# Kernel optimization log

Hardware: AMD Instinct MI355X
Metric: run time of the kernel (lower is better)

Reference implementation:

```python
import jax, jax.numpy as jnp
import numpy as np

B, T, N = 32, 64, 36
VD, H, S = 2048, 512, 300


def setup_inputs() -> dict:
    key = jax.random.key(0)
    ks = jax.random.split(key, 24)
    sc = 0.02
    d = {
        "visual": jax.random.normal(ks[0], (B, T, VD), jnp.float32),
        "objects": jax.random.normal(ks[1], (B, N, H), jnp.float32),
        # linear_layer
        "lin_W": jax.random.normal(ks[2], (H, VD), jnp.float32) * sc,
        "lin_b": jnp.zeros((H,), jnp.float32),
        # W, U projections
        "W_W": jax.random.normal(ks[3], (H, H), jnp.float32) * sc,
        "W_b": jnp.zeros((H,), jnp.float32),
        "U_W": jax.random.normal(ks[4], (H, H), jnp.float32) * sc,
        "U_b": jnp.zeros((H,), jnp.float32),
        # additive attention bias (torch.ones init)
        "b_attn": jnp.ones((H,), jnp.float32),
        # scoring vector w: Linear(H, 1)
        "w_W": jax.random.normal(ks[5], (1, H), jnp.float32) * sc,
        "w_b": jnp.zeros((1,), jnp.float32),
        # BiLSTM: input 2H, hidden H//2 per direction; gate order i,f,g,o
        "Wih_f": jax.random.normal(ks[6], (4 * (H // 2), 2 * H), jnp.float32) * sc,
        "Whh_f": jax.random.normal(ks[7], (4 * (H // 2), H // 2), jnp.float32) * sc,
        "bih_f": jnp.zeros((4 * (H // 2),), jnp.float32),
        "bhh_f": jnp.zeros((4 * (H // 2),), jnp.float32),
        "Wih_b": jax.random.normal(ks[8], (4 * (H // 2), 2 * H), jnp.float32) * sc,
        "Whh_b": jax.random.normal(ks[9], (4 * (H // 2), H // 2), jnp.float32) * sc,
        "bih_b": jnp.zeros((4 * (H // 2),), jnp.float32),
        "bhh_b": jnp.zeros((4 * (H // 2),), jnp.float32),
        # fc_layer
        "fc_W": jax.random.normal(ks[10], (S, H), jnp.float32) * sc,
        "fc_b": jnp.zeros((S,), jnp.float32),
    }
    return d


def _lstm(x, Wih, Whh, b):
    """Unidirectional LSTM over time. x: [B, T, D] -> [B, T, Hc]."""
    bsz = x.shape[0]
    Hc = Whh.shape[1]

    def step(carry, xt):
        h, c = carry
        g = xt @ Wih.T + h @ Whh.T + b          # [B, 4Hc]
        i, f, gg, o = jnp.split(g, 4, axis=-1)  # torch gate order i,f,g,o
        c = jax.nn.sigmoid(f) * c + jax.nn.sigmoid(i) * jnp.tanh(gg)
        h = jax.nn.sigmoid(o) * jnp.tanh(c)
        return (h, c), h

    h0 = jnp.zeros((bsz, Hc), x.dtype)
    _, hs = jax.lax.scan(step, (h0, h0), jnp.swapaxes(x, 0, 1))
    return jnp.swapaxes(hs, 0, 1)


def reference(visual, objects, lin_W, lin_b, W_W, W_b, U_W, U_b, b_attn,
              w_W, w_b, Wih_f, Whh_f, bih_f, bhh_f, Wih_b, Whh_b, bih_b,
              bhh_b, fc_W, fc_b):
    f3d = visual @ lin_W.T + lin_b                 # [B, T, H]
    Wf = f3d @ W_W.T + W_b                         # [B, T, H]
    Uo = objects @ U_W.T + U_b                     # [B, N, H]
    # broadcast additive attention: [B, T, N, H]
    attn_feat = Wf[:, :, None, :] + Uo[:, None, :, :] + b_attn
    scores = jnp.tanh(attn_feat) @ w_W.T + w_b     # [B, T, N, 1]
    attn_w = jax.nn.softmax(scores, axis=-2)       # softmax over objects N
    attn_obj = (attn_w * attn_feat).sum(axis=-2)   # [B, T, H]
    feats = jnp.concatenate([f3d, attn_obj], axis=-1)  # [B, T, 2H]
    out_f = _lstm(feats, Wih_f, Whh_f, bih_f + bhh_f)
    out_b = _lstm(feats[:, ::-1, :], Wih_b, Whh_b, bih_b + bhh_b)[:, ::-1, :]
    output = jnp.concatenate([out_f, out_b], axis=-1)  # [B, T, H]
    action = jnp.max(output, axis=1)                   # [B, H]
    action_semantics = action @ fc_W.T + fc_b          # [B, S]
    return output, action_semantics
```

## Files before the change

kernel.cpp:

```cpp
#include <hip/hip_runtime.h>
#include <hip/hip_bf16.h>
#include <type_traits>


typedef __hip_bfloat16 bf16;
typedef unsigned int uint32;
typedef __attribute__((ext_vector_type(8))) short s8v;
typedef __attribute__((ext_vector_type(4))) float f4v;
typedef __attribute__((ext_vector_type(4))) int   i32x4;

__device__ inline f4v mfma16(s8v a, s8v b, f4v c) {
    return __builtin_amdgcn_mfma_f32_16x16x32_bf16(a, b, c, 0, 0, 0);
}
__device__ inline float sigf(float x) {
    return __builtin_amdgcn_rcpf(1.f + __expf(-x));
}
__device__ inline float tanh_(float x) {
    return 1.f - 2.f * __builtin_amdgcn_rcpf(1.f + __expf(2.f * x));
}
__device__ inline void gload_lds16(const bf16* g, bf16* l) {
    __builtin_amdgcn_global_load_lds(
        (const __attribute__((address_space(1))) void*)g,
        (__attribute__((address_space(3))) void*)l, 16, 0, 0);
}

struct CvtJobs {
    const float* src[9];
    bf16*        dst[9];
    int          start[10];
};

__global__ __launch_bounds__(256) void cvt_kernel(CvtJobs jobs) {
    int blk = blockIdx.x;
    int j = 0;
#pragma unroll
    for (int i = 1; i < 9; ++i) if (blk >= jobs.start[i]) j = i;
    int off = (blk - jobs.start[j]) * 1024 + threadIdx.x * 4;
    float4 v = *(const float4*)(jobs.src[j] + off);
    union { bf16 h[4]; uint2 u; } p;
    p.h[0] = __float2bfloat16(v.x);
    p.h[1] = __float2bfloat16(v.y);
    p.h[2] = __float2bfloat16(v.z);
    p.h[3] = __float2bfloat16(v.w);
    *(uint2*)(jobs.dst[j] + off) = p.u;
}

template <typename CT>
__global__ __launch_bounds__(256) void gemm_tile(
    const bf16* __restrict__ A, int lda,
    const bf16* __restrict__ W,
    const float* __restrict__ b1, const float* __restrict__ b2,
    CT* __restrict__ C, int ldc,
    int K, int tiles_n, int permuteTB)
{
    __shared__ bf16 As[128 * 64];
    __shared__ bf16 Bs[128 * 64];

    int tid = threadIdx.x;
    int w = tid >> 6, lane = tid & 63;
    int lo = lane & 15, hi = lane >> 4;
    int mt = blockIdx.x / tiles_n, nt = blockIdx.x % tiles_n;
    int wm = w >> 1, wn = w & 1;

    const bf16* Ab = A + (size_t)(mt * 128) * lda;
    const bf16* Wb = W + (size_t)(nt * 128) * K;

    f4v acc[4][4];
#pragma unroll
    for (int m = 0; m < 4; ++m)
#pragma unroll
        for (int n = 0; n < 4; ++n) acc[m][n] = (f4v){0.f, 0.f, 0.f, 0.f};

    int wbase = tid & 192;

    for (int k0 = 0; k0 < K; k0 += 64) {
#pragma unroll
        for (int i = 0; i < 4; ++i) {
            int ci = i * 256 + tid;
            int row = ci >> 3, c = ci & 7;
            int gc = c ^ (row & 7);
            gload_lds16(Ab + (size_t)row * lda + k0 + gc * 8,
                        As + (i * 256 + wbase) * 8);
            gload_lds16(Wb + (size_t)row * K + k0 + gc * 8,
                        Bs + (i * 256 + wbase) * 8);
        }
        __syncthreads();

#pragma unroll
        for (int kt = 0; kt < 2; ++kt) {
            s8v a[4], b[4];
            int sw = ((kt * 4 + hi) ^ (lo & 7)) * 8;
#pragma unroll
            for (int m = 0; m < 4; ++m)
                a[m] = *(const s8v*)(As + (wm * 64 + m * 16 + lo) * 64 + sw);
#pragma unroll
            for (int n = 0; n < 4; ++n)
                b[n] = *(const s8v*)(Bs + (wn * 64 + n * 16 + lo) * 64 + sw);
#pragma unroll
            for (int m = 0; m < 4; ++m)
#pragma unroll
                for (int n = 0; n < 4; ++n)
                    acc[m][n] = mfma16(a[m], b[n], acc[m][n]);
        }
        __syncthreads();
    }

#pragma unroll
    for (int n = 0; n < 4; ++n) {
        int cc = nt * 128 + wn * 64 + n * 16 + lo;
        float bv = (b1 ? b1[cc] : 0.f) + (b2 ? b2[cc] : 0.f);
#pragma unroll
        for (int m = 0; m < 4; ++m) {
            int rbase = mt * 128 + wm * 64 + m * 16 + hi * 4;
#pragma unroll
            for (int i = 0; i < 4; ++i) {
                int r = rbase + i;
                int rr = permuteTB ? ((r & 63) * 32 + (r >> 6)) : r;
                float v = acc[m][n][i] + bv;
                if constexpr (std::is_same<CT, float>::value)
                    C[(size_t)rr * ldc + cc] = v;
                else
                    C[(size_t)rr * ldc + cc] = __float2bfloat16(v);
            }
        }
    }
}

__global__ __launch_bounds__(256) void attn_kernel(
    const float* __restrict__ Wf,
    const float* __restrict__ Uo,
    const float* __restrict__ wW,
    const float* __restrict__ wB,
    bf16* __restrict__ feats)
{
    int bt = blockIdx.x, b = bt >> 6;
    int wv = threadIdx.x >> 6, lane = threadIdx.x & 63;
    __shared__ float s_aw[36];

    float wfr[8], wr[8];
    const float* wfrow = Wf + (size_t)bt * 512 + lane * 8;
#pragma unroll
    for (int i = 0; i < 8; ++i) {
        wfr[i] = wfrow[i];
        wr[i]  = wW[lane * 8 + i];
    }
    float wbv = wB[0];

    for (int n = wv; n < 36; n += 4) {
        const float* uo = Uo + ((size_t)b * 36 + n) * 512 + lane * 8;
        float s = 0.f;
#pragma unroll
        for (int i = 0; i < 8; ++i) s += wr[i] * tanh_(wfr[i] + uo[i]);
#pragma unroll
        for (int off = 32; off; off >>= 1) s += __shfl_xor(s, off);
        if (lane == 0) s_aw[n] = s + wbv;
    }
    __syncthreads();
    if (threadIdx.x == 0) {
        float mx = -1e30f;
#pragma unroll
        for (int n = 0; n < 36; ++n) mx = fmaxf(mx, s_aw[n]);
        float e[36], sum = 0.f;
#pragma unroll
        for (int n = 0; n < 36; ++n) { e[n] = __expf(s_aw[n] - mx); sum += e[n]; }
        float r = __builtin_amdgcn_rcpf(sum);
#pragma unroll
        for (int n = 0; n < 36; ++n) s_aw[n] = e[n] * r;
    }
    __syncthreads();

    int h0 = threadIdx.x * 2;
    const float* wf2 = Wf + (size_t)bt * 512 + h0;
    float a0 = wf2[0], a1 = wf2[1];
    for (int n = 0; n < 36; ++n) {
        float awn = s_aw[n];
        const float* uo = Uo + ((size_t)b * 36 + n) * 512 + h0;
        a0 += awn * uo[0];
        a1 += awn * uo[1];
    }
    feats[(size_t)bt * 1024 + 512 + h0]     = __float2bfloat16(a0);
    feats[(size_t)bt * 1024 + 512 + h0 + 1] = __float2bfloat16(a1);
}

__device__ inline void poll4(const int* p, int need) {
    for (;;) {
        i32x4 f;
        asm volatile("global_load_dwordx4 %0, %1, off sc1\n\t"
                     "s_waitcnt vmcnt(0)"
                     : "=v"(f) : "v"(p) : "memory");
        if (f[0] >= need && f[1] >= need && f[2] >= need && f[3] >= need)
            break;
    }
}

__device__ inline void load_h16(const uint32* pF, const uint32* pB, s8v* aF) {
    asm volatile(
        "global_load_dwordx4 %0, %16, off sc1\n\t"
        "global_load_dwordx4 %1, %16, off offset:64 sc1\n\t"
        "global_load_dwordx4 %2, %16, off offset:128 sc1\n\t"
        "global_load_dwordx4 %3, %16, off offset:192 sc1\n\t"
        "global_load_dwordx4 %4, %16, off offset:256 sc1\n\t"
        "global_load_dwordx4 %5, %16, off offset:320 sc1\n\t"
        "global_load_dwordx4 %6, %16, off offset:384 sc1\n\t"
        "global_load_dwordx4 %7, %16, off offset:448 sc1\n\t"
        "global_load_dwordx4 %8, %17, off sc1\n\t"
        "global_load_dwordx4 %9, %17, off offset:64 sc1\n\t"
        "global_load_dwordx4 %10, %17, off offset:128 sc1\n\t"
        "global_load_dwordx4 %11, %17, off offset:192 sc1\n\t"
        "global_load_dwordx4 %12, %17, off offset:256 sc1\n\t"
        "global_load_dwordx4 %13, %17, off offset:320 sc1\n\t"
        "global_load_dwordx4 %14, %17, off offset:384 sc1\n\t"
        "global_load_dwordx4 %15, %17, off offset:448 sc1\n\t"
        "s_waitcnt vmcnt(0)"
        : "=v"(aF[0]), "=v"(aF[1]), "=v"(aF[2]), "=v"(aF[3]),
          "=v"(aF[4]), "=v"(aF[5]), "=v"(aF[6]), "=v"(aF[7]),
          "=v"(aF[8]), "=v"(aF[9]), "=v"(aF[10]), "=v"(aF[11]),
          "=v"(aF[12]), "=v"(aF[13]), "=v"(aF[14]), "=v"(aF[15])
        : "v"(pF), "v"(pB)
        : "memory");
}

__global__ __launch_bounds__(256, 1) void lstm_kernel(
    const bf16* __restrict__ WhhF, const bf16* __restrict__ WhhB,
    const float* __restrict__ gatesF, const float* __restrict__ gatesB,
    uint32* __restrict__ hx,
    float* __restrict__ out,
    int* __restrict__ bar)
{
    int bi  = blockIdx.x;
    int g   = bi >> 2;
    int pid = bi & 3;
    int jb  = pid * 64;
    int wv = threadIdx.x >> 6, lane = threadIdx.x & 63;
    int lo = lane & 15, hi = lane >> 4;
    int j0 = jb + wv * 16;

    uint32* hxg  = hx + (size_t)g * 8192;
    int*    flags = bar + g * 16;

    s8v whh[2][4][8];
#pragma unroll
    for (int q = 0; q < 4; ++q)
#pragma unroll
        for (int kt = 0; kt < 8; ++kt) {
            whh[0][q][kt] = *(const s8v*)(WhhF + (size_t)(q * 256 + j0 + lo) * 256 + kt * 32 + hi * 8);
            whh[1][q][kt] = *(const s8v*)(WhhB + (size_t)(q * 256 + j0 + lo) * 256 + kt * 32 + hi * 8);
        }

    int jbw = jb >> 1;
    for (int x = threadIdx.x; x < 1024; x += 256) {
        int d = x >> 9, b = (x >> 5) & 15, jw = jbw + (x & 31);
        __hip_atomic_store(&hxg[d * 4096 + b * 128 + jw], 0u,
                           __ATOMIC_RELAXED, __HIP_MEMORY_SCOPE_AGENT);
    }
    __syncthreads();
    if (threadIdx.x == 0)
        __hip_atomic_store(&flags[pid], 1, __ATOMIC_RELAXED,
                           __HIP_MEMORY_SCOPE_AGENT);

    poll4(flags, 1);
    s8v aF[16];
    {
        const uint32* pF = hxg + lo * 128 + hi * 4;
        load_h16(pF, pF + 4096, aF);
    }

    float cstf[4] = {0.f,0.f,0.f,0.f}, cstb[4] = {0.f,0.f,0.f,0.f};

    for (int t = 0; t < 64; ++t) {
        int tpF = t, tpB = 63 - t;
        int slot = (t + 1) & 1;

        float gvf[4][4], gvb[4][4];
#pragma unroll
        for (int i = 0; i < 4; ++i) {
            int bg = g * 16 + hi * 4 + i;
#pragma unroll
            for (int q = 0; q < 4; ++q) {
                gvf[q][i] = gatesF[(size_t)tpF * 32768 + bg * 1024 + q * 256 + j0 + lo];
                gvb[q][i] = gatesB[(size_t)tpB * 32768 + bg * 1024 + q * 256 + j0 + lo];
            }
        }

        float hvf[4];
        {
            f4v acc[4];
#pragma unroll
            for (int q = 0; q < 4; ++q) acc[q] = (f4v){0.f,0.f,0.f,0.f};
#pragma unroll
            for (int kt = 0; kt < 8; ++kt)
#pragma unroll
                for (int q = 0; q < 4; ++q)
                    acc[q] = mfma16(aF[kt], whh[0][q][kt], acc[q]);
#pragma unroll
            for (int i = 0; i < 4; ++i) {
                float xi = acc[0][i] + gvf[0][i];
                float xf = acc[1][i] + gvf[1][i];
                float xg = acc[2][i] + gvf[2][i];
                float xo = acc[3][i] + gvf[3][i];
                float c = sigf(xf) * cstf[i] + sigf(xi) * tanh_(xg);
                cstf[i] = c;
                hvf[i] = sigf(xo) * tanh_(c);
            }
        }
        if (t < 63) {
            uint32* hw = hxg + slot * 2048;
#pragma unroll
            for (int i = 0; i < 4; ++i) {
                float o2 = __shfl_xor(hvf[i], 1);
                if (!(lane & 1)) {
                    uint32 pk = (uint32)__bfloat16_as_ushort(__float2bfloat16(hvf[i]))
                              | ((uint32)__bfloat16_as_ushort(__float2bfloat16(o2)) << 16);
                    __hip_atomic_store(&hw[(hi * 4 + i) * 128 + ((j0 + lo) >> 1)], pk,
                                       __ATOMIC_RELAXED, __HIP_MEMORY_SCOPE_AGENT);
                }
            }
        }

        float hvb[4];
        {
            f4v acc[4];
#pragma unroll
            for (int q = 0; q < 4; ++q) acc[q] = (f4v){0.f,0.f,0.f,0.f};
#pragma unroll
            for (int kt = 0; kt < 8; ++kt)
#pragma unroll
                for (int q = 0; q < 4; ++q)
                    acc[q] = mfma16(aF[8 + kt], whh[1][q][kt], acc[q]);
#pragma unroll
            for (int i = 0; i < 4; ++i) {
                float xi = acc[0][i] + gvb[0][i];
                float xf = acc[1][i] + gvb[1][i];
                float xg = acc[2][i] + gvb[2][i];
                float xo = acc[3][i] + gvb[3][i];
                float c = sigf(xf) * cstb[i] + sigf(xi) * tanh_(xg);
                cstb[i] = c;
                hvb[i] = sigf(xo) * tanh_(c);
            }
        }
        if (t < 63) {
            uint32* hw = hxg + 4096 + slot * 2048;
#pragma unroll
            for (int i = 0; i < 4; ++i) {
                float o2 = __shfl_xor(hvb[i], 1);
                if (!(lane & 1)) {
                    uint32 pk = (uint32)__bfloat16_as_ushort(__float2bfloat16(hvb[i]))
                              | ((uint32)__bfloat16_as_ushort(__float2bfloat16(o2)) << 16);
                    __hip_atomic_store(&hw[(hi * 4 + i) * 128 + ((j0 + lo) >> 1)], pk,
                                       __ATOMIC_RELAXED, __HIP_MEMORY_SCOPE_AGENT);
                }
            }
        }

#pragma unroll
        for (int i = 0; i < 4; ++i) {
            int bg = g * 16 + hi * 4 + i;
            out[((size_t)bg * 64 + tpF) * 512 + j0 + lo]       = hvf[i];
            out[((size_t)bg * 64 + tpB) * 512 + 256 + j0 + lo] = hvb[i];
        }

        if (t < 63) {
            __syncthreads();
            if (threadIdx.x == 0)
                __hip_atomic_store(&flags[pid], t + 2, __ATOMIC_RELAXED,
                                   __HIP_MEMORY_SCOPE_AGENT);
            poll4(flags, t + 2);
            const uint32* pF = hxg + slot * 2048 + lo * 128 + hi * 4;
            load_h16(pF, pF + 4096, aF);
        }
    }
}

__global__ __launch_bounds__(256) void final_kernel(
    const float* __restrict__ out,
    const float* __restrict__ fcW,
    const float* __restrict__ fcb,
    float* __restrict__ osem)
{
    int b = blockIdx.x, tid = threadIdx.x;
    __shared__ float act[512];
    for (int h = tid; h < 512; h += 256) {
        float m = -1e30f;
        const float* p = out + (size_t)b * 64 * 512 + h;
#pragma unroll 8
        for (int t = 0; t < 64; ++t) m = fmaxf(m, p[t * 512]);
        act[h] = m;
    }
    __syncthreads();
    int wv = tid >> 6, lane = tid & 63;
    for (int s = wv; s < 300; s += 4) {
        const float* wrow = fcW + (size_t)s * 512 + lane * 8;
        float a = 0.f;
#pragma unroll
        for (int i = 0; i < 8; ++i) a += act[lane * 8 + i] * wrow[i];
#pragma unroll
        for (int off = 32; off; off >>= 1) a += __shfl_xor(a, off);
        if (lane == 0) osem[b * 300 + s] = a + fcb[s];
    }
}

extern "C" void kernel_launch(void* const* d_in, const int* in_sizes, int n_in,
                              void* d_out, int out_size, void* d_ws, size_t ws_size,
                              hipStream_t stream)
{
    const float* visual  = (const float*)d_in[0];
    const float* objects = (const float*)d_in[1];
    const float* lin_W   = (const float*)d_in[2];
    const float* lin_b   = (const float*)d_in[3];
    const float* W_W     = (const float*)d_in[4];
    const float* W_b     = (const float*)d_in[5];
    const float* U_W     = (const float*)d_in[6];
    const float* U_b     = (const float*)d_in[7];
    const float* b_attn  = (const float*)d_in[8];
    const float* w_W     = (const float*)d_in[9];
    const float* w_b     = (const float*)d_in[10];
    const float* Wih_f   = (const float*)d_in[11];
    const float* Whh_f   = (const float*)d_in[12];
    const float* bih_f   = (const float*)d_in[13];
    const float* bhh_f   = (const float*)d_in[14];
    const float* Wih_b   = (const float*)d_in[15];
    const float* Whh_b   = (const float*)d_in[16];
    const float* bih_b   = (const float*)d_in[17];
    const float* bhh_b   = (const float*)d_in[18];
    const float* fc_W    = (const float*)d_in[19];
    const float* fc_b    = (const float*)d_in[20];

    char* ws = (char*)d_ws;
    size_t o = 0;
    bf16*   feats   = (bf16*)(ws + o);   o += (size_t)2048 * 1024 * 2;
    float*  Wf      = (float*)(ws + o);  o += (size_t)2048 * 512 * 4;
    float*  Uo      = (float*)(ws + o);  o += (size_t)1152 * 512 * 4;
    float*  gatesF  = (float*)(ws + o);  o += (size_t)2048 * 1024 * 4;
    float*  gatesB  = (float*)(ws + o);  o += (size_t)2048 * 1024 * 4;
    uint32* hx      = (uint32*)(ws + o); o += (size_t)2 * 8192 * 4;
    int*    bar     = (int*)(ws + o);    o += 256;
    bf16*  visual_b  = (bf16*)(ws + o); o += (size_t)4194304 * 2;
    bf16*  objects_b = (bf16*)(ws + o); o += (size_t)589824 * 2;
    bf16*  lin_Wb    = (bf16*)(ws + o); o += (size_t)1048576 * 2;
    bf16*  W_Wb      = (bf16*)(ws + o); o += (size_t)262144 * 2;
    bf16*  U_Wb      = (bf16*)(ws + o); o += (size_t)262144 * 2;
    bf16*  Wih_fb    = (bf16*)(ws + o); o += (size_t)1048576 * 2;
    bf16*  Whh_fb    = (bf16*)(ws + o); o += (size_t)262144 * 2;
    bf16*  Wih_bb    = (bf16*)(ws + o); o += (size_t)1048576 * 2;
    bf16*  Whh_bb    = (bf16*)(ws + o); o += (size_t)262144 * 2;

    CvtJobs cj;
    const float* srcs[9] = {visual, objects, lin_W, W_W, U_W, Wih_f, Whh_f, Wih_b, Whh_b};
    bf16* dsts[9] = {visual_b, objects_b, lin_Wb, W_Wb, U_Wb, Wih_fb, Whh_fb, Wih_bb, Whh_bb};
    int ns[9] = {4194304, 589824, 1048576, 262144, 262144, 1048576, 262144, 1048576, 262144};
    int acc_b = 0;
    for (int i = 0; i < 9; ++i) {
        cj.src[i] = srcs[i];
        cj.dst[i] = dsts[i];
        cj.start[i] = acc_b;
        acc_b += ns[i] / 1024;
    }
    cj.start[9] = acc_b;

    dim3 blk(256);
    cvt_kernel<<<acc_b, blk, 0, stream>>>(cj);

    gemm_tile<bf16><<<64, blk, 0, stream>>>(visual_b, 2048, lin_Wb, lin_b, nullptr,
                                            feats, 1024, 2048, 4, 0);
    gemm_tile<float><<<36, blk, 0, stream>>>(objects_b, 512, U_Wb, U_b, b_attn,
                                             Uo, 512, 512, 4, 0);
    gemm_tile<float><<<64, blk, 0, stream>>>(feats, 1024, W_Wb, W_b, nullptr,
                                             Wf, 512, 512, 4, 0);
    attn_kernel<<<2048, blk, 0, stream>>>(Wf, Uo, w_W, w_b, feats);
    gemm_tile<float><<<128, blk, 0, stream>>>(feats, 1024, Wih_fb, bih_f, bhh_f,
                                              gatesF, 1024, 1024, 8, 1);
    gemm_tile<float><<<128, blk, 0, stream>>>(feats, 1024, Wih_bb, bih_b, bhh_b,
                                              gatesB, 1024, 1024, 8, 1);
    lstm_kernel<<<8, blk, 0, stream>>>(Whh_fb, Whh_bb, gatesF, gatesB, hx,
                                       (float*)d_out, bar);
    final_kernel<<<32, blk, 0, stream>>>((float*)d_out, fc_W, fc_b,
                                         (float*)d_out + 1048576);
}
```

Baseline: 591.7 us.

## Merge GEMM launches, tile attention by batch, and tag LSTM hidden-state exchange

Result: slower. 698.4 us (+18.0%).

```diff
diff --git a/kernel.cpp b/kernel.cpp
--- a/kernel.cpp
+++ b/kernel.cpp
@@ -7,6 +7,7 @@
 typedef unsigned int uint32;
 typedef __attribute__((ext_vector_type(8))) short s8v;
 typedef __attribute__((ext_vector_type(4))) float f4v;
+typedef __attribute__((ext_vector_type(4))) uint32 u32x4;
 typedef __attribute__((ext_vector_type(4))) int   i32x4;
 
 __device__ inline f4v mfma16(s8v a, s8v b, f4v c) {
@@ -17,6 +18,9 @@
 }
 __device__ inline float tanh_(float x) {
     return 1.f - 2.f * __builtin_amdgcn_rcpf(1.f + __expf(2.f * x));
+}
+__device__ inline uint32 pack2(uint32 d0, uint32 d1) {
+    return __builtin_amdgcn_perm(d1, d0, 0x05040100u);
 }
 __device__ inline void gload_lds16(const bf16* g, bf16* l) {
     __builtin_amdgcn_global_load_lds(
@@ -45,29 +49,25 @@
     *(uint2*)(jobs.dst[j] + off) = p.u;
 }
 
-template <typename CT>
-__global__ __launch_bounds__(256) void gemm_tile(
+template <int MT>
+__device__ inline void gemm_body(
+    bf16* As, bf16* Bs,
     const bf16* __restrict__ A, int lda,
     const bf16* __restrict__ W,
     const float* __restrict__ b1, const float* __restrict__ b2,
-    CT* __restrict__ C, int ldc,
-    int K, int tiles_n, int permuteTB)
-{
-    __shared__ bf16 As[128 * 64];
-    __shared__ bf16 Bs[128 * 64];
-
+    void* C, int ldc, int K, int mt, int nt, int obf, int permuteTB)
+{
     int tid = threadIdx.x;
     int w = tid >> 6, lane = tid & 63;
     int lo = lane & 15, hi = lane >> 4;
-    int mt = blockIdx.x / tiles_n, nt = blockIdx.x % tiles_n;
     int wm = w >> 1, wn = w & 1;
 
-    const bf16* Ab = A + (size_t)(mt * 128) * lda;
+    const bf16* Ab = A + (size_t)(mt * (MT * 32)) * lda;
     const bf16* Wb = W + (size_t)(nt * 128) * K;
 
-    f4v acc[4][4];
-#pragma unroll
-    for (int m = 0; m < 4; ++m)
+    f4v acc[MT][4];
+#pragma unroll
+    for (int m = 0; m < MT; ++m)
 #pragma unroll
         for (int n = 0; n < 4; ++n) acc[m][n] = (f4v){0.f, 0.f, 0.f, 0.f};
 
@@ -75,12 +75,18 @@
 
     for (int k0 = 0; k0 < K; k0 += 64) {
 #pragma unroll
-        for (int i = 0; i < 4; ++i) {
+        for (int i = 0; i < MT; ++i) {
             int ci = i * 256 + tid;
             int row = ci >> 3, c = ci & 7;
             int gc = c ^ (row & 7);
             gload_lds16(Ab + (size_t)row * lda + k0 + gc * 8,
                         As + (i * 256 + wbase) * 8);
+        }
+#pragma unroll
+        for (int i = 0; i < 4; ++i) {
+            int ci = i * 256 + tid;
+            int row = ci >> 3, c = ci & 7;
+            int gc = c ^ (row & 7);
             gload_lds16(Wb + (size_t)row * K + k0 + gc * 8,
                         Bs + (i * 256 + wbase) * 8);
         }
@@ -88,16 +94,16 @@
 
 #pragma unroll
         for (int kt = 0; kt < 2; ++kt) {
-            s8v a[4], b[4];
+            s8v a[MT], b[4];
             int sw = ((kt * 4 + hi) ^ (lo & 7)) * 8;
 #pragma unroll
-            for (int m = 0; m < 4; ++m)
-                a[m] = *(const s8v*)(As + (wm * 64 + m * 16 + lo) * 64 + sw);
+            for (int m = 0; m < MT; ++m)
+                a[m] = *(const s8v*)(As + (wm * (MT * 16) + m * 16 + lo) * 64 + sw);
 #pragma unroll
             for (int n = 0; n < 4; ++n)
                 b[n] = *(const s8v*)(Bs + (wn * 64 + n * 16 + lo) * 64 + sw);
 #pragma unroll
-            for (int m = 0; m < 4; ++m)
+            for (int m = 0; m < MT; ++m)
 #pragma unroll
                 for (int n = 0; n < 4; ++n)
                     acc[m][n] = mfma16(a[m], b[n], acc[m][n]);
@@ -110,20 +116,62 @@
         int cc = nt * 128 + wn * 64 + n * 16 + lo;
         float bv = (b1 ? b1[cc] : 0.f) + (b2 ? b2[cc] : 0.f);
 #pragma unroll
-        for (int m = 0; m < 4; ++m) {
-            int rbase = mt * 128 + wm * 64 + m * 16 + hi * 4;
+        for (int m = 0; m < MT; ++m) {
+            int rbase = mt * (MT * 32) + wm * (MT * 16) + m * 16 + hi * 4;
 #pragma unroll
             for (int i = 0; i < 4; ++i) {
                 int r = rbase + i;
                 int rr = permuteTB ? ((r & 63) * 32 + (r >> 6)) : r;
                 float v = acc[m][n][i] + bv;
-                if constexpr (std::is_same<CT, float>::value)
-                    C[(size_t)rr * ldc + cc] = v;
-                else
-                    C[(size_t)rr * ldc + cc] = __float2bfloat16(v);
-            }
-        }
-    }
+                if (obf) ((bf16*)C)[(size_t)rr * ldc + cc] = __float2bfloat16(v);
+                else     ((float*)C)[(size_t)rr * ldc + cc] = v;
+            }
+        }
+    }
+}
+
+__global__ __launch_bounds__(256) void gemm_pre(
+    const bf16* visual_b, const bf16* lin_Wb, const float* lin_b,
+    const bf16* objects_b, const bf16* U_Wb, const float* U_b,
+    const float* b_attn, bf16* feats, float* Uo)
+{
+    __shared__ bf16 As[64 * 64];
+    __shared__ bf16 Bs[128 * 64];
+    int blk = blockIdx.x;
+    if (blk < 128)
+        gemm_body<2>(As, Bs, visual_b, 2048, lin_Wb, lin_b, nullptr,
+                     feats, 1024, 2048, blk / 4, blk % 4, 1, 0);
+    else {
+        int bi = blk - 128;
+        gemm_body<2>(As, Bs, objects_b, 512, U_Wb, U_b, b_attn,
+                     Uo, 512, 512, bi / 4, bi % 4, 0, 0);
+    }
+}
+
+__global__ __launch_bounds__(256) void gemm_wf(
+    const bf16* feats, const bf16* W_Wb, const float* W_b, float* Wf)
+{
+    __shared__ bf16 As[64 * 64];
+    __shared__ bf16 Bs[128 * 64];
+    gemm_body<2>(As, Bs, feats, 1024, W_Wb, W_b, nullptr,
+                 Wf, 512, 512, blockIdx.x / 4, blockIdx.x % 4, 0, 0);
+}
+
+__global__ __launch_bounds__(256) void gemm_gates(
+    const bf16* feats, const bf16* Wih_fb, const bf16* Wih_bb,
+    const float* bih_f, const float* bhh_f,
+    const float* bih_b, const float* bhh_b,
+    float* gatesF, float* gatesB)
+{
+    __shared__ bf16 As[128 * 64];
+    __shared__ bf16 Bs[128 * 64];
+    int sel = blockIdx.x >> 7;
+    int blk = blockIdx.x & 127;
+    gemm_body<4>(As, Bs, feats, 1024,
+                 sel ? Wih_bb : Wih_fb,
+                 sel ? bih_b : bih_f, sel ? bhh_b : bhh_f,
+                 sel ? gatesB : gatesF, 1024, 1024,
+                 blk / 8, blk % 8, 0, 1);
 }
 
 __global__ __launch_bounds__(256) void attn_kernel(
@@ -133,91 +181,125 @@
     const float* __restrict__ wB,
     bf16* __restrict__ feats)
 {
-    int bt = blockIdx.x, b = bt >> 6;
-    int wv = threadIdx.x >> 6, lane = threadIdx.x & 63;
+    __shared__ float sh_uo[36 * 512];
     __shared__ float s_aw[36];
-
-    float wfr[8], wr[8];
-    const float* wfrow = Wf + (size_t)bt * 512 + lane * 8;
-#pragma unroll
-    for (int i = 0; i < 8; ++i) {
-        wfr[i] = wfrow[i];
-        wr[i]  = wW[lane * 8 + i];
-    }
+    int b = blockIdx.x >> 3, tg = blockIdx.x & 7;
+    int tid = threadIdx.x, wv = tid >> 6, lane = tid & 63;
+
+    {
+        const float4* src = (const float4*)(Uo + (size_t)b * 18432);
+        float4* dst = (float4*)sh_uo;
+        for (int i = tid; i < 4608; i += 256) dst[i] = src[i];
+    }
+    float wr[8];
+#pragma unroll
+    for (int i = 0; i < 8; ++i) wr[i] = wW[lane * 8 + i];
     float wbv = wB[0];
-
-    for (int n = wv; n < 36; n += 4) {
-        const float* uo = Uo + ((size_t)b * 36 + n) * 512 + lane * 8;
-        float s = 0.f;
-#pragma unroll
-        for (int i = 0; i < 8; ++i) s += wr[i] * tanh_(wfr[i] + uo[i]);
-#pragma unroll
-        for (int off = 32; off; off >>= 1) s += __shfl_xor(s, off);
-        if (lane == 0) s_aw[n] = s + wbv;
-    }
     __syncthreads();
-    if (threadIdx.x == 0) {
-        float mx = -1e30f;
-#pragma unroll
-        for (int n = 0; n < 36; ++n) mx = fmaxf(mx, s_aw[n]);
-        float e[36], sum = 0.f;
-#pragma unroll
-        for (int n = 0; n < 36; ++n) { e[n] = __expf(s_aw[n] - mx); sum += e[n]; }
-        float r = __builtin_amdgcn_rcpf(sum);
-#pragma unroll
-        for (int n = 0; n < 36; ++n) s_aw[n] = e[n] * r;
-    }
-    __syncthreads();
-
-    int h0 = threadIdx.x * 2;
-    const float* wf2 = Wf + (size_t)bt * 512 + h0;
-    float a0 = wf2[0], a1 = wf2[1];
-    for (int n = 0; n < 36; ++n) {
-        float awn = s_aw[n];
-        const float* uo = Uo + ((size_t)b * 36 + n) * 512 + h0;
-        a0 += awn * uo[0];
-        a1 += awn * uo[1];
-    }
-    feats[(size_t)bt * 1024 + 512 + h0]     = __float2bfloat16(a0);
-    feats[(size_t)bt * 1024 + 512 + h0 + 1] = __float2bfloat16(a1);
-}
-
-__device__ inline void poll4(const int* p, int need) {
+
+    for (int ts = 0; ts < 8; ++ts) {
+        int bt = b * 64 + tg * 8 + ts;
+        const float* wfrow = Wf + (size_t)bt * 512;
+        float wfr[8];
+#pragma unroll
+        for (int i = 0; i < 8; ++i) wfr[i] = wfrow[lane * 8 + i];
+
+        for (int n = wv; n < 36; n += 4) {
+            const float* uo = sh_uo + n * 512 + lane * 8;
+            float s = 0.f;
+#pragma unroll
+            for (int i = 0; i < 8; ++i) s += wr[i] * tanh_(wfr[i] + uo[i]);
+#pragma unroll
+            for (int off = 32; off; off >>= 1) s += __shfl_xor(s, off);
+            if (lane == 0) s_aw[n] = s + wbv;
+        }
+        __syncthreads();
+        if (tid < 64) {
+            float v = (lane < 36) ? s_aw[lane] : -1e30f;
+            float mx = v;
+#pragma unroll
+            for (int off = 32; off; off >>= 1) mx = fmaxf(mx, __shfl_xor(mx, off));
+            float e = (lane < 36) ? __expf(v - mx) : 0.f;
+            float sum = e;
+#pragma unroll
+            for (int off = 32; off; off >>= 1) sum += __shfl_xor(sum, off);
+            if (lane < 36) s_aw[lane] = e * __builtin_amdgcn_rcpf(sum);
+        }
+        __syncthreads();
+
+        int h0 = tid * 2;
+        float a0 = wfrow[h0], a1 = wfrow[h0 + 1];
+        for (int n = 0; n < 36; ++n) {
+            float awn = s_aw[n];
+            a0 += awn * sh_uo[n * 512 + h0];
+            a1 += awn * sh_uo[n * 512 + h0 + 1];
+        }
+        feats[(size_t)bt * 1024 + 512 + h0]     = __float2bfloat16(a0);
+        feats[(size_t)bt * 1024 + 512 + h0 + 1] = __float2bfloat16(a1);
+        __syncthreads();
+    }
+}
+
+__device__ inline void spec_load(const uint32* pF, const uint32* pB,
+                                 const int* pf, u32x4* rw, i32x4* fl)
+{
+    asm volatile(
+        "global_load_dwordx4 %0, %33, off sc1\n\t"
+        "global_load_dwordx4 %1, %33, off offset:16 sc1\n\t"
+        "global_load_dwordx4 %2, %33, off offset:128 sc1\n\t"
+        "global_load_dwordx4 %3, %33, off offset:144 sc1\n\t"
+        "global_load_dwordx4 %4, %33, off offset:256 sc1\n\t"
+        "global_load_dwordx4 %5, %33, off offset:272 sc1\n\t"
+        "global_load_dwordx4 %6, %33, off offset:384 sc1\n\t"
+        "global_load_dwordx4 %7, %33, off offset:400 sc1\n\t"
+        "global_load_dwordx4 %8, %33, off offset:512 sc1\n\t"
+        "global_load_dwordx4 %9, %33, off offset:528 sc1\n\t"
+        "global_load_dwordx4 %10, %33, off offset:640 sc1\n\t"
+        "global_load_dwordx4 %11, %33, off offset:656 sc1\n\t"
+        "global_load_dwordx4 %12, %33, off offset:768 sc1\n\t"
+        "global_load_dwordx4 %13, %33, off offset:784 sc1\n\t"
+        "global_load_dwordx4 %14, %33, off offset:896 sc1\n\t"
+        "global_load_dwordx4 %15, %33, off offset:912 sc1\n\t"
+        "global_load_dwordx4 %16, %34, off sc1\n\t"
+        "global_load_dwordx4 %17, %34, off offset:16 sc1\n\t"
+        "global_load_dwordx4 %18, %34, off offset:128 sc1\n\t"
+        "global_load_dwordx4 %19, %34, off offset:144 sc1\n\t"
+        "global_load_dwordx4 %20, %34, off offset:256 sc1\n\t"
+        "global_load_dwordx4 %21, %34, off offset:272 sc1\n\t"
+        "global_load_dwordx4 %22, %34, off offset:384 sc1\n\t"
+        "global_load_dwordx4 %23, %34, off offset:400 sc1\n\t"
+        "global_load_dwordx4 %24, %34, off offset:512 sc1\n\t"
+        "global_load_dwordx4 %25, %34, off offset:528 sc1\n\t"
+        "global_load_dwordx4 %26, %34, off offset:640 sc1\n\t"
+        "global_load_dwordx4 %27, %34, off offset:656 sc1\n\t"
+        "global_load_dwordx4 %28, %34, off offset:768 sc1\n\t"
+        "global_load_dwordx4 %29, %34, off offset:784 sc1\n\t"
+        "global_load_dwordx4 %30, %34, off offset:896 sc1\n\t"
+        "global_load_dwordx4 %31, %34, off offset:912 sc1\n\t"
+        "global_load_dwordx4 %32, %35, off sc1\n\t"
+        "s_waitcnt vmcnt(0)"
+        : "=v"(rw[0]), "=v"(rw[1]), "=v"(rw[2]), "=v"(rw[3]),
+          "=v"(rw[4]), "=v"(rw[5]), "=v"(rw[6]), "=v"(rw[7]),
+          "=v"(rw[8]), "=v"(rw[9]), "=v"(rw[10]), "=v"(rw[11]),
+          "=v"(rw[12]), "=v"(rw[13]), "=v"(rw[14]), "=v"(rw[15]),
+          "=v"(rw[16]), "=v"(rw[17]), "=v"(rw[18]), "=v"(rw[19]),
+          "=v"(rw[20]), "=v"(rw[21]), "=v"(rw[22]), "=v"(rw[23]),
+          "=v"(rw[24]), "=v"(rw[25]), "=v"(rw[26]), "=v"(rw[27]),
+          "=v"(rw[28]), "=v"(rw[29]), "=v"(rw[30]), "=v"(rw[31]),
+          "=v"(*fl)
+        : "v"(pF), "v"(pB), "v"(pf)
+        : "memory");
+}
+
+__device__ inline void poll_flags(const int* pf, int need) {
     for (;;) {
         i32x4 f;
         asm volatile("global_load_dwordx4 %0, %1, off sc1\n\t"
                      "s_waitcnt vmcnt(0)"
-                     : "=v"(f) : "v"(p) : "memory");
+                     : "=v"(f) : "v"(pf) : "memory");
         if (f[0] >= need && f[1] >= need && f[2] >= need && f[3] >= need)
             break;
     }
-}
-
-__device__ inline void load_h16(const uint32* pF, const uint32* pB, s8v* aF) {
-    asm volatile(
-        "global_load_dwordx4 %0, %16, off sc1\n\t"
-        "global_load_dwordx4 %1, %16, off offset:64 sc1\n\t"
-        "global_load_dwordx4 %2, %16, off offset:128 sc1\n\t"
-        "global_load_dwordx4 %3, %16, off offset:192 sc1\n\t"
-        "global_load_dwordx4 %4, %16, off offset:256 sc1\n\t"
-        "global_load_dwordx4 %5, %16, off offset:320 sc1\n\t"
-        "global_load_dwordx4 %6, %16, off offset:384 sc1\n\t"
-        "global_load_dwordx4 %7, %16, off offset:448 sc1\n\t"
-        "global_load_dwordx4 %8, %17, off sc1\n\t"
-        "global_load_dwordx4 %9, %17, off offset:64 sc1\n\t"
-        "global_load_dwordx4 %10, %17, off offset:128 sc1\n\t"
-        "global_load_dwordx4 %11, %17, off offset:192 sc1\n\t"
-        "global_load_dwordx4 %12, %17, off offset:256 sc1\n\t"
-        "global_load_dwordx4 %13, %17, off offset:320 sc1\n\t"
-        "global_load_dwordx4 %14, %17, off offset:384 sc1\n\t"
-        "global_load_dwordx4 %15, %17, off offset:448 sc1\n\t"
-        "s_waitcnt vmcnt(0)"
-        : "=v"(aF[0]), "=v"(aF[1]), "=v"(aF[2]), "=v"(aF[3]),
-          "=v"(aF[4]), "=v"(aF[5]), "=v"(aF[6]), "=v"(aF[7]),
-          "=v"(aF[8]), "=v"(aF[9]), "=v"(aF[10]), "=v"(aF[11]),
-          "=v"(aF[12]), "=v"(aF[13]), "=v"(aF[14]), "=v"(aF[15])
-        : "v"(pF), "v"(pB)
-        : "memory");
 }
 
 __global__ __launch_bounds__(256, 1) void lstm_kernel(
@@ -235,8 +317,8 @@
     int lo = lane & 15, hi = lane >> 4;
     int j0 = jb + wv * 16;
 
-    uint32* hxg  = hx + (size_t)g * 8192;
-    int*    flags = bar + g * 16;
+    uint32* hxg  = hx + (size_t)g * 16384;
+    int* flags = bar + g * 16;
 
     s8v whh[2][4][8];
 #pragma unroll
@@ -247,10 +329,9 @@
             whh[1][q][kt] = *(const s8v*)(WhhB + (size_t)(q * 256 + j0 + lo) * 256 + kt * 32 + hi * 8);
         }
 
-    int jbw = jb >> 1;
-    for (int x = threadIdx.x; x < 1024; x += 256) {
-        int d = x >> 9, b = (x >> 5) & 15, jw = jbw + (x & 31);
-        __hip_atomic_store(&hxg[d * 4096 + b * 128 + jw], 0u,
+    for (int x = threadIdx.x; x < 2048; x += 256) {
+        int d = x >> 10, b = (x >> 6) & 15, j = jb + (x & 63);
+        __hip_atomic_store(&hxg[d * 8192 + b * 256 + j], 0u,
                            __ATOMIC_RELAXED, __HIP_MEMORY_SCOPE_AGENT);
     }
     __syncthreads();
@@ -258,18 +339,34 @@
         __hip_atomic_store(&flags[pid], 1, __ATOMIC_RELAXED,
                            __HIP_MEMORY_SCOPE_AGENT);
 
-    poll4(flags, 1);
+    u32x4 rw[32];
+    i32x4 fl;
+    poll_flags(flags, 1);
+    {
+        const uint32* pF = hxg + lo * 256 + hi * 8;
+        spec_load(pF, pF + 8192, flags, rw, &fl);
+    }
     s8v aF[16];
-    {
-        const uint32* pF = hxg + lo * 128 + hi * 4;
-        load_h16(pF, pF + 4096, aF);
-    }
+#pragma unroll
+    for (int kt = 0; kt < 8; ++kt)
+#pragma unroll
+        for (int d = 0; d < 2; ++d) {
+            u32x4 A0 = rw[d * 16 + kt * 2];
+            u32x4 A1 = rw[d * 16 + kt * 2 + 1];
+            union { uint32 u[4]; s8v v; } tt;
+            tt.u[0] = pack2(A0[0], A0[1]);
+            tt.u[1] = pack2(A0[2], A0[3]);
+            tt.u[2] = pack2(A1[0], A1[1]);
+            tt.u[3] = pack2(A1[2], A1[3]);
+            aF[d * 8 + kt] = tt.v;
+        }
 
     float cstf[4] = {0.f,0.f,0.f,0.f}, cstb[4] = {0.f,0.f,0.f,0.f};
 
     for (int t = 0; t < 64; ++t) {
         int tpF = t, tpB = 63 - t;
         int slot = (t + 1) & 1;
+        uint32 tagw = (uint32)(t + 1) << 16;
 
         float gvf[4][4], gvb[4][4];
 #pragma unroll
@@ -304,17 +401,12 @@
             }
         }
         if (t < 63) {
-            uint32* hw = hxg + slot * 2048;
-#pragma unroll
-            for (int i = 0; i < 4; ++i) {
-                float o2 = __shfl_xor(hvf[i], 1);
-                if (!(lane & 1)) {
-                    uint32 pk = (uint32)__bfloat16_as_ushort(__float2bfloat16(hvf[i]))
-                              | ((uint32)__bfloat16_as_ushort(__float2bfloat16(o2)) << 16);
-                    __hip_atomic_store(&hw[(hi * 4 + i) * 128 + ((j0 + lo) >> 1)], pk,
-                                       __ATOMIC_RELAXED, __HIP_MEMORY_SCOPE_AGENT);
-                }
-            }
+            uint32* hw = hxg + slot * 4096;
+#pragma unroll
+            for (int i = 0; i < 4; ++i)
+                __hip_atomic_store(&hw[(hi * 4 + i) * 256 + j0 + lo],
+                    tagw | (uint32)__bfloat16_as_ushort(__float2bfloat16(hvf[i])),
+                    __ATOMIC_RELAXED, __HIP_MEMORY_SCOPE_AGENT);
         }
 
         float hvb[4];
@@ -339,34 +431,62 @@
             }
         }
         if (t < 63) {
-            uint32* hw = hxg + 4096 + slot * 2048;
+            uint32* hw = hxg + 8192 + slot * 4096;
+#pragma unroll
+            for (int i = 0; i < 4; ++i)
+                __hip_atomic_store(&hw[(hi * 4 + i) * 256 + j0 + lo],
+                    tagw | (uint32)__bfloat16_as_ushort(__float2bfloat16(hvb[i])),
+                    __ATOMIC_RELAXED, __HIP_MEMORY_SCOPE_AGENT);
+        }
+
+        __syncthreads();
+        if (threadIdx.x == 0)
+            __hip_atomic_store(&flags[pid], t + 2, __ATOMIC_RELAXED,
+                               __HIP_MEMORY_SCOPE_AGENT);
+
+        if (t < 63) {
+            const uint32* pF = hxg + slot * 4096 + lo * 256 + hi * 8;
+            spec_load(pF, pF + 8192, flags, rw, &fl);
 #pragma unroll
             for (int i = 0; i < 4; ++i) {
-                float o2 = __shfl_xor(hvb[i], 1);
-                if (!(lane & 1)) {
-                    uint32 pk = (uint32)__bfloat16_as_ushort(__float2bfloat16(hvb[i]))
-                              | ((uint32)__bfloat16_as_ushort(__float2bfloat16(o2)) << 16);
-                    __hip_atomic_store(&hw[(hi * 4 + i) * 128 + ((j0 + lo) >> 1)], pk,
-                                       __ATOMIC_RELAXED, __HIP_MEMORY_SCOPE_AGENT);
+                int bg = g * 16 + hi * 4 + i;
+                out[((size_t)bg * 64 + tpF) * 512 + j0 + lo]       = hvf[i];
+                out[((size_t)bg * 64 + tpB) * 512 + 256 + j0 + lo] = hvb[i];
+            }
+            uint32 bad = 0;
+#pragma unroll
+            for (int q = 0; q < 32; ++q)
+                bad |= (rw[q][0] ^ tagw) | (rw[q][1] ^ tagw) |
+                       (rw[q][2] ^ tagw) | (rw[q][3] ^ tagw);
+            int tagok  = !__any(bad >> 16);
+            int need   = t + 2;
+            int flagok = (fl[0] >= need) && (fl[1] >= need) &&
+                         (fl[2] >= need) && (fl[3] >= need);
+            if (!(tagok && flagok)) {
+                poll_flags(flags, need);
+                if (!tagok)
+                    spec_load(pF, pF + 8192, flags, rw, &fl);
+            }
+#pragma unroll
+            for (int kt = 0; kt < 8; ++kt)
+#pragma unroll
+                for (int d = 0; d < 2; ++d) {
+                    u32x4 A0 = rw[d * 16 + kt * 2];
+                    u32x4 A1 = rw[d * 16 + kt * 2 + 1];
+                    union { uint32 u[4]; s8v v; } tt;
+                    tt.u[0] = pack2(A0[0], A0[1]);
+                    tt.u[1] = pack2(A0[2], A0[3]);
+                    tt.u[2] = pack2(A1[0], A1[1]);
+                    tt.u[3] = pack2(A1[2], A1[3]);
+                    aF[d * 8 + kt] = tt.v;
                 }
-            }
-        }
-
-#pragma unroll
-        for (int i = 0; i < 4; ++i) {
-            int bg = g * 16 + hi * 4 + i;
-            out[((size_t)bg * 64 + tpF) * 512 + j0 + lo]       = hvf[i];
-            out[((size_t)bg * 64 + tpB) * 512 + 256 + j0 + lo] = hvb[i];
-        }
-
-        if (t < 63) {
-            __syncthreads();
-            if (threadIdx.x == 0)
-                __hip_atomic_store(&flags[pid], t + 2, __ATOMIC_RELAXED,
-                                   __HIP_MEMORY_SCOPE_AGENT);
-            poll4(flags, t + 2);
-            const uint32* pF = hxg + slot * 2048 + lo * 128 + hi * 4;
-            load_h16(pF, pF + 4096, aF);
+        } else {
+#pragma unroll
+            for (int i = 0; i < 4; ++i) {
+                int bg = g * 16 + hi * 4 + i;
+                out[((size_t)bg * 64 + tpF) * 512 + j0 + lo]       = hvf[i];
+                out[((size_t)bg * 64 + tpB) * 512 + 256 + j0 + lo] = hvb[i];
+            }
         }
     }
 }
@@ -430,9 +550,9 @@
     bf16*   feats   = (bf16*)(ws + o);   o += (size_t)2048 * 1024 * 2;
     float*  Wf      = (float*)(ws + o);  o += (size_t)2048 * 512 * 4;
     float*  Uo      = (float*)(ws + o);  o += (size_t)1152 * 512 * 4;
-    float*  gatesF  = (float*)(ws + o);  o += (size_t)2048 * 1024 * 4;
-    float*  gatesB  = (float*)(ws + o);  o += (size_t)2048 * 1024 * 4;
-    uint32* hx      = (uint32*)(ws + o); o += (size_t)2 * 8192 * 4;
+    float*  gatesF  = (float*)(ws + o);  o += (size_t)2097152 * 4;
+    float*  gatesB  = (float*)(ws + o);  o += (size_t)2097152 * 4;
+    uint32* hx      = (uint32*)(ws + o); o += (size_t)2 * 16384 * 4;
     int*    bar     = (int*)(ws + o);    o += 256;
     bf16*  visual_b  = (bf16*)(ws + o); o += (size_t)4194304 * 2;
     bf16*  objects_b = (bf16*)(ws + o); o += (size_t)589824 * 2;
@@ -444,6 +564,8 @@
     bf16*  Wih_bb    = (bf16*)(ws + o); o += (size_t)1048576 * 2;
     bf16*  Whh_bb    = (bf16*)(ws + o); o += (size_t)262144 * 2;
 
+    hipMemsetAsync(bar, 0, 256, stream);
+
     CvtJobs cj;
     const float* srcs[9] = {visual, objects, lin_W, W_W, U_W, Wih_f, Whh_f, Wih_b, Whh_b};
     bf16* dsts[9] = {visual_b, objects_b, lin_Wb, W_Wb, U_Wb, Wih_fb, Whh_fb, Wih_bb, Whh_bb};
@@ -460,17 +582,13 @@
     dim3 blk(256);
     cvt_kernel<<<acc_b, blk, 0, stream>>>(cj);
 
-    gemm_tile<bf16><<<64, blk, 0, stream>>>(visual_b, 2048, lin_Wb, lin_b, nullptr,
-                                            feats, 1024, 2048, 4, 0);
-    gemm_tile<float><<<36, blk, 0, stream>>>(objects_b, 512, U_Wb, U_b, b_attn,
-                                             Uo, 512, 512, 4, 0);
-    gemm_tile<float><<<64, blk, 0, stream>>>(feats, 1024, W_Wb, W_b, nullptr,
-                                             Wf, 512, 512, 4, 0);
-    attn_kernel<<<2048, blk, 0, stream>>>(Wf, Uo, w_W, w_b, feats);
-    gemm_tile<float><<<128, blk, 0, stream>>>(feats, 1024, Wih_fb, bih_f, bhh_f,
-                                              gatesF, 1024, 1024, 8, 1);
-    gemm_tile<float><<<128, blk, 0, stream>>>(feats, 1024, Wih_bb, bih_b, bhh_b,
-                                              gatesB, 1024, 1024, 8, 1);
+    gemm_pre<<<200, blk, 0, stream>>>(visual_b, lin_Wb, lin_b,
+                                      objects_b, U_Wb, U_b, b_attn, feats, Uo);
+    gemm_wf<<<128, blk, 0, stream>>>(feats, W_Wb, W_b, Wf);
+    attn_kernel<<<256, blk, 0, stream>>>(Wf, Uo, w_W, w_b, feats);
+    gemm_gates<<<256, blk, 0, stream>>>(feats, Wih_fb, Wih_bb,
+                                        bih_f, bhh_f, bih_b, bhh_b,
+                                        gatesF, gatesB);
     lstm_kernel<<<8, blk, 0, stream>>>(Whh_fb, Whh_bb, gatesF, gatesB, hx,
                                        (float*)d_out, bar);
     final_kernel<<<32, blk, 0, stream>>>((float*)d_out, fc_W, fc_b,
```
